# Optimization experiments

Measured on AMD Instinct MI355X. Metric: run time of the kernel, lower is better.

## Reference

```python
import jax, jax.numpy as jnp
import numpy as np

W_BLEND, L1, L2, L3 = 0.5, 0.3, 0.3, 0.4
B, S, F, H, C = 64, 256, 256, 1024, 256


def setup_inputs() -> dict:
    key = jax.random.key(0)
    ks = jax.random.split(key, 11)
    sc = 0.05  # keep recurrence numerically tame
    return {
        "x": jax.random.normal(ks[0], (B, S, F), jnp.float32),
        "W_ih0": jax.random.normal(ks[1], (4 * H, 2 * F), jnp.float32) * sc,
        "W_hh0": jax.random.normal(ks[2], (4 * H, H), jnp.float32) * sc,
        "b_ih0": jax.random.normal(ks[3], (4 * H,), jnp.float32) * sc,
        "b_hh0": jax.random.normal(ks[4], (4 * H,), jnp.float32) * sc,
        "W_ih1": jax.random.normal(ks[5], (4 * H, H), jnp.float32) * sc,
        "W_hh1": jax.random.normal(ks[6], (4 * H, H), jnp.float32) * sc,
        "b_ih1": jax.random.normal(ks[7], (4 * H,), jnp.float32) * sc,
        "b_hh1": jax.random.normal(ks[8], (4 * H,), jnp.float32) * sc,
        "fc_W": jax.random.normal(ks[9], (C, H), jnp.float32) * sc,
        "fc_b": jax.random.normal(ks[10], (C,), jnp.float32) * sc,
    }


def _lstm_cell(inp, h, c, W_ih, W_hh, b_ih, b_hh):
    # PyTorch gate order: i, f, g, o
    gates = inp @ W_ih.T + h @ W_hh.T + b_ih + b_hh  # [B, 4H]
    i, f, g, o = jnp.split(gates, 4, axis=-1)
    i, f, o = jax.nn.sigmoid(i), jax.nn.sigmoid(f), jax.nn.sigmoid(o)
    g = jnp.tanh(g)
    c_new = f * c + i * g
    h_new = o * jnp.tanh(c_new)
    return h_new, c_new


def reference(x, W_ih0, W_hh0, b_ih0, b_hh0, W_ih1, W_hh1, b_ih1, b_hh1, fc_W, fc_b):
    Bx = x.shape[0]
    denom = 1.0 + W_BLEND * (L1 + L2 + L3)
    h0 = jnp.zeros((Bx, H), x.dtype)
    c0 = jnp.zeros((Bx, H), x.dtype)
    action0 = jnp.zeros((Bx, F), x.dtype)

    def step(carry, inputs):
        h0_, c0_, h1_, c1_, action = carry
        x_t, idx = inputs  # x_t: [B, F]
        inp = jnp.concatenate([x_t, action], axis=-1)  # [B, 2F]
        h0n, c0n = _lstm_cell(inp, h0_, c0_, W_ih0, W_hh0, b_ih0, b_hh0)
        h1n, c1n = _lstm_cell(h0n, h1_, c1_, W_ih1, W_hh1, b_ih1, b_hh1)
        out = h1n @ fc_W.T + fc_b  # [B, C] == [B, F]
        blend = ((1.0 + W_BLEND * L2) * x_t + W_BLEND * L1 * action
                 + W_BLEND * L3 * out) / denom
        new_action = jnp.where(idx < 1, x_t, blend)
        return (h0n, c0n, h1n, c1n, new_action), new_action

    xs = (jnp.swapaxes(x, 0, 1), jnp.arange(x.shape[1]))  # ([S,B,F], [S])
    _, actions = jax.lax.scan(step, (h0, c0, h0, c0, action0), xs)
    return jnp.swapaxes(actions, 0, 1)  # [B, S, F]
```

## Files before the change

kernel.cpp:

```cpp
#include <hip/hip_runtime.h>

#define B_ 64
#define S_ 256
#define F_ 256
#define H_ 1024

typedef __attribute__((ext_vector_type(8))) short bf16x8;
typedef __attribute__((ext_vector_type(4))) float f32x4;
typedef unsigned long long u64;

#define MFMA(a, b, c) __builtin_amdgcn_mfma_f32_16x16x32_bf16(a, b, c, 0, 0, 0)
#define CBAR() asm volatile("" ::: "memory")

__device__ __forceinline__ float sig(float v) { return 1.0f / (1.0f + __expf(-v)); }
__device__ __forceinline__ float tanh_(float v) { return 1.0f - 2.0f / (__expf(2.0f * v) + 1.0f); }
__device__ __forceinline__ short bfr(float f) {
    unsigned u = __float_as_uint(f);
    u += 0x7fffu + ((u >> 16) & 1u);
    return (short)(u >> 16);
}

__device__ __forceinline__ void st4(short* base, size_t byteoff, unsigned v) {
    __hip_atomic_store((unsigned*)((char*)base + byteoff), v,
                       __ATOMIC_RELAXED, __HIP_MEMORY_SCOPE_AGENT);
}

__device__ __forceinline__ void flag_add(unsigned* line) {
    asm volatile("s_waitcnt vmcnt(0)" ::: "memory");
    __hip_atomic_fetch_add(line, 1u, __ATOMIC_RELAXED, __HIP_MEMORY_SCOPE_AGENT);
}

__device__ __forceinline__ void flag_wait_g(unsigned* lines, int lane31, unsigned tgt) {
    for (;;) {
        unsigned s = __hip_atomic_load(&lines[lane31 * 16], __ATOMIC_RELAXED,
                                       __HIP_MEMORY_SCOPE_AGENT);
        s += __shfl_xor(s, 1);
        s += __shfl_xor(s, 2);
        s += __shfl_xor(s, 4);
        s += __shfl_xor(s, 8);
        s += __shfl_xor(s, 16);
        if (s >= tgt) break;
        __builtin_amdgcn_s_sleep(1);
    }
    CBAR();
}

__device__ __forceinline__ void rel_wait(unsigned* f, unsigned tgt) {
    while (__hip_atomic_load(f, __ATOMIC_RELAXED, __HIP_MEMORY_SCOPE_AGENT) < tgt)
        __builtin_amdgcn_s_sleep(1);
    CBAR();
}

__device__ __forceinline__ void tok_spin(volatile unsigned* tk, unsigned v) {
    while (*tk < v) __builtin_amdgcn_s_sleep(1);
    CBAR();
}

__global__ __launch_bounds__(256) void conv_x(const float* __restrict__ x,
                                              short* __restrict__ xbf) {
    int tid = blockIdx.x * 256 + threadIdx.x;
    int lane = tid & 63;
    int m = (tid >> 6) & 3;
    int kf = (tid >> 8) & 7;
    int t = tid >> 11;
    int b = m * 16 + (lane & 15);
    int kb = kf * 32 + (lane >> 4) * 8;
    const float* src = x + ((size_t)b * S_ + t) * F_ + kb;
    float4 v0 = *(const float4*)src, v1 = *(const float4*)(src + 4);
    bf16x8 o;
    o[0] = bfr(v0.x); o[1] = bfr(v0.y); o[2] = bfr(v0.z); o[3] = bfr(v0.w);
    o[4] = bfr(v1.x); o[5] = bfr(v1.y); o[6] = bfr(v1.z); o[7] = bfr(v1.w);
    *(bf16x8*)(xbf + (size_t)tid * 8) = o;
}

__global__ void zero_f(float* __restrict__ p, int n) {
    int i = blockIdx.x * blockDim.x + threadIdx.x;
    if (i < n) p[i] = 0.0f;
}

__global__ __launch_bounds__(256) void precomp(const float* __restrict__ Wih0,
                                               const float* __restrict__ fcW,
                                               const float* __restrict__ fcb,
                                               short* __restrict__ Mf,
                                               float* __restrict__ c0ws) {
    __shared__ float WaL[16][256];
    const int nf = blockIdx.x, tid = threadIdx.x;
    #pragma unroll
    for (int r = 0; r < 16; ++r) {
        int rowp = nf * 16 + r;
        int up = rowp >> 2, gat = rowp & 3;
        WaL[r][tid] = Wih0[(size_t)(gat * H_ + up) * 512 + 256 + tid];
    }
    __syncthreads();
    f32x4 acc[16];
    #pragma unroll
    for (int r = 0; r < 16; ++r) acc[r] = (f32x4){0, 0, 0, 0};
    for (int c = 0; c < 256; ++c) {
        f32x4 wv = *(const f32x4*)&fcW[(size_t)c * 1024 + tid * 4];
        #pragma unroll
        for (int r = 0; r < 16; ++r) acc[r] += WaL[r][c] * wv;
    }
    #pragma unroll
    for (int r = 0; r < 16; ++r) {
        #pragma unroll
        for (int jj = 0; jj < 4; ++jj) {
            int h = tid * 4 + jj;
            int kf = h >> 5;
            int lane = r + ((h >> 3) & 3) * 16;
            int j = h & 7;
            Mf[((size_t)nf * 32 + kf) * 512 + lane * 8 + j] = bfr(acc[r][jj]);
        }
    }
    if (tid < 16) {
        float s = 0.0f;
        for (int c = 0; c < 256; ++c) s += WaL[tid][c] * fcb[c];
        c0ws[nf * 16 + tid] = s;
    }
}

#define GATES(v)                                                        \
    float x1 = __shfl_xor((v), 1), x2 = __shfl_xor((v), 2), x3 = __shfl_xor((v), 3); \
    float aL = g1 ? x1 : (v), aH = g1 ? x3 : x2;                        \
    float bL = g1 ? (v) : x1, bH = g1 ? x2 : x3;                        \
    float i_ = g2 ? aH : aL;                                            \
    float f_ = g2 ? bH : bL;                                            \
    float gc = g2 ? aL : aH;                                            \
    float o_ = g2 ? bL : bH;                                            \
    i_ = sig(i_); f_ = sig(f_); o_ = sig(o_); gc = tanh_(gc);

__global__ __launch_bounds__(512, 1) void persist(
    const float* __restrict__ Wih0, const float* __restrict__ Whh0,
    const float* __restrict__ bih0, const float* __restrict__ bhh0,
    const float* __restrict__ Wih1, const float* __restrict__ Whh1,
    const float* __restrict__ bih1, const float* __restrict__ bhh1,
    const float* __restrict__ fcW,  const float* __restrict__ fcb,
    const float* __restrict__ x,    const short* __restrict__ xbf,
    short* __restrict__ h0S, short* __restrict__ h1S,
    const short* __restrict__ Mf, const float* __restrict__ c0ws,
    float* __restrict__ outp,
    unsigned* __restrict__ flagA, unsigned* __restrict__ flagB,
    unsigned* __restrict__ relA,  unsigned* __restrict__ relB)
{
    __shared__ f32x4 redGA[2048];
    __shared__ f32x4 redBv[2048];
    __shared__ f32x4 redDv[2048];
    __shared__ f32x4 fcF[256];
    __shared__ short ldsC[16384];
    __shared__ unsigned tokA, tokB;
    const int tid = threadIdx.x, lane = tid & 63, w = tid >> 6;
    const int nf = blockIdx.x;
    const int lane31 = lane & 31;
    unsigned* lineA = &flagA[(nf >> 3) * 16];
    unsigned* lineB = &flagB[(nf >> 3) * 16];
    unsigned* myRelA = &relA[(nf >> 5) * 16];
    unsigned* myRelB = &relB[(nf >> 5) * 16];
    const int rowp = nf * 16 + (lane & 15);
    const int up = rowp >> 2, g = rowp & 3;
    const int g1 = lane & 1, g2 = lane & 2;
    const f32x4 zero4 = {0, 0, 0, 0};
    const int chunkA = (nf >> 3) * 4 + w;
    const int lsBase = ((nf & 7) >> 1) * 16;
    const int pb = (nf & 1) * 4 + ((lane & 15) >> 3) * 2;
    const int mfc = nf >> 4;

    if (tid == 0) { tokA = 0; tokB = 0; }

    bf16x8 wA0, waQ, wH[8], wX[8];
    {
        int k = w * 32 + (lane >> 4) * 8;
        const float* src = Wih0 + (size_t)(g * H_ + up) * 512 + k;
        #pragma unroll
        for (int j = 0; j < 8; ++j) wA0[j] = bfr(src[j]);
    }
    {
        int k = 256 + w * 32 + (lane >> 4) * 8;
        const float* src = Wih0 + (size_t)(g * H_ + up) * 512 + k;
        #pragma unroll
        for (int j = 0; j < 8; ++j) waQ[j] = bfr(src[j]);
    }
    if (w < 4) {
        #pragma unroll
        for (int i = 0; i < 8; ++i) {
            int k = (w * 8 + i) * 32 + (lane >> 4) * 8;
            const float* sh = Whh0 + (size_t)(g * H_ + up) * 1024 + k;
            const float* sx = Wih1 + (size_t)(g * H_ + up) * 1024 + k;
            #pragma unroll
            for (int j = 0; j < 8; ++j) { wH[i][j] = bfr(sh[j]); wX[i][j] = bfr(sx[j]); }
        }
    } else {
        #pragma unroll
        for (int i = 0; i < 8; ++i) {
            int k = ((w - 4) * 8 + i) * 32 + (lane >> 4) * 8;
            const float* sh = Whh1 + (size_t)(g * H_ + up) * 1024 + k;
            #pragma unroll
            for (int j = 0; j < 8; ++j) wH[i][j] = bfr(sh[j]);
            wX[i] = *(const bf16x8*)(Mf + ((size_t)nf * 32 + (w - 4) * 8 + i) * 512 + lane * 8);
        }
    }
    const float bias0 = bih0[g * H_ + up] + bhh0[g * H_ + up];
    const float bias1 = bih1[g * H_ + up] + bhh1[g * H_ + up];
    const float c0l = c0ws[nf * 16 + (lane & 15)];
    float biasC = 0.0f;
    if (nf < 64) {
        int rowc = (nf & 15) * 16 + (lane & 15);
        biasC = fcb[rowc];
        #pragma unroll
        for (int i = 0; i < 4; ++i) {
            int kf = w * 4 + i;
            int k = kf * 32 + (lane >> 4) * 8;
            const float* src = fcW + (size_t)rowc * 1024 + k;
            short* d = ldsC + ((size_t)kf * 64 + lane) * 8;
            #pragma unroll
            for (int j = 0; j < 8; ++j) d[j] = bfr(src[j]);
        }
    }
    __syncthreads();

    float cs0[4] = {0, 0, 0, 0}, cs1[4] = {0, 0, 0, 0};
    float areg[4] = {0, 0, 0, 0}, P[4] = {0, 0, 0, 0};

    f32x4 ga0, ga1, ga2, ga3, q0, q1, q2, q3;
    f32x4 qp0 = zero4, qp1 = zero4, qp2 = zero4, qp3 = zero4;
    {
        const short* p = xbf + (size_t)w * 2048 + lane * 8;
        bf16x8 a0 = *(const bf16x8*)(p);
        bf16x8 a1 = *(const bf16x8*)(p + 512);
        bf16x8 a2 = *(const bf16x8*)(p + 1024);
        bf16x8 a3 = *(const bf16x8*)(p + 1536);
        ga0 = MFMA(a0, wA0, zero4);  ga1 = MFMA(a1, wA0, zero4);
        ga2 = MFMA(a2, wA0, zero4);  ga3 = MFMA(a3, wA0, zero4);
        q0 = MFMA(a0, waQ, zero4);  q1 = MFMA(a1, waQ, zero4);
        q2 = MFMA(a2, waQ, zero4);  q3 = MFMA(a3, waQ, zero4);
    }

    for (int t = 0; t < S_; ++t) {
        const unsigned ut = (unsigned)t;
        short* h0w = h0S + (size_t)t * 65536;
        const short* h1r = h1S + (size_t)t * 65536;
        short* h1w = h1S + (size_t)(t + 1) * 65536;

        if (w == 0) {
            if (t > 0) {
                if (nf == 0) {
                    flag_wait_g(flagB, lane31, 256u * ut);
                    if (lane < 8)
                        __hip_atomic_store(&relB[lane * 16], ut,
                                           __ATOMIC_RELAXED, __HIP_MEMORY_SCOPE_AGENT);
                } else {
                    rel_wait(myRelB, ut);
                }
                if (lane == 0) *(volatile unsigned*)&tokB = ut;
                CBAR();
            }
        } else if (w >= 4 && t > 0) {
            tok_spin(&tokB, ut);
        }
        redGA[(w * 4 + 0) * 64 + lane] = ga0;
        redGA[(w * 4 + 1) * 64 + lane] = ga1;
        redGA[(w * 4 + 2) * 64 + lane] = ga2;
        redGA[(w * 4 + 3) * 64 + lane] = ga3;
        f32x4 m0 = zero4, m1 = zero4, m2 = zero4, m3 = zero4;
        if (w >= 4) {
            f32x4 b0 = zero4, b1 = zero4, b2 = zero4, b3 = zero4;
            #pragma unroll
            for (int i = 0; i < 8; ++i) {
                const short* p = h1r + (size_t)((w - 4) * 8 + i) * 2048 + lane * 8;
                bf16x8 a0 = *(const bf16x8*)(p);
                bf16x8 a1 = *(const bf16x8*)(p + 512);
                bf16x8 a2 = *(const bf16x8*)(p + 1024);
                bf16x8 a3 = *(const bf16x8*)(p + 1536);
                if (t > 1) {
                    m0 = MFMA(a0, wX[i], m0);
                    m1 = MFMA(a1, wX[i], m1);
                    m2 = MFMA(a2, wX[i], m2);
                    m3 = MFMA(a3, wX[i], m3);
                }
                b0 = MFMA(a0, wH[i], b0);
                b1 = MFMA(a1, wH[i], b1);
                b2 = MFMA(a2, wH[i], b2);
                b3 = MFMA(a3, wH[i], b3);
            }
            redBv[(w * 4 + 0) * 64 + lane] = b0;
            redBv[(w * 4 + 1) * 64 + lane] = b1;
            redBv[(w * 4 + 2) * 64 + lane] = b2;
            redBv[(w * 4 + 3) * 64 + lane] = b3;
        }
        if (t > 0) {
            f32x4 R0, R1, R2, R3;
            if (t == 1) { R0 = qp0; R1 = qp1; R2 = qp2; R3 = qp3; }
            else if (w >= 4) {
                R0 = 1.15f * qp0 + 0.2f * m0;
                R1 = 1.15f * qp1 + 0.2f * m1;
                R2 = 1.15f * qp2 + 0.2f * m2;
                R3 = 1.15f * qp3 + 0.2f * m3;
            } else {
                R0 = 1.15f * qp0; R1 = 1.15f * qp1; R2 = 1.15f * qp2; R3 = 1.15f * qp3;
            }
            redDv[(w * 4 + 0) * 64 + lane] = R0;
            redDv[(w * 4 + 1) * 64 + lane] = R1;
            redDv[(w * 4 + 2) * 64 + lane] = R2;
            redDv[(w * 4 + 3) * 64 + lane] = R3;
        }
        __syncthreads();

        if (w < 4) {
            if (t > 0) {
                f32x4 sD = redDv[(0 * 4 + w) * 64 + lane];
                #pragma unroll
                for (int k = 1; k < 8; ++k) sD += redDv[(k * 4 + w) * 64 + lane];
                #pragma unroll
                for (int r = 0; r < 4; ++r)
                    P[r] = (t == 1) ? sD[r]
                         : (sD[r] + 0.15f * P[r] + 0.2f * c0l) * (1.0f / 1.5f);
            }
            f32x4 s = redGA[(0 * 4 + w) * 64 + lane];
            #pragma unroll
            for (int k = 1; k < 8; ++k) s += redGA[(k * 4 + w) * 64 + lane];
            #pragma unroll
            for (int r = 0; r < 4; ++r) {
                float v = s[r] + bias0 + P[r];
                GATES(v)
                float cn = f_ * cs0[r] + i_ * gc;
                cs0[r] = cn;
                float hn = o_ * tanh_(cn);
                int hv = (int)(unsigned short)bfr(hn);
                int ot = __shfl_xor(hv, 4);
                unsigned p32 = (lane & 4) ? (unsigned)((ot & 0xffff) | (hv << 16))
                                          : (unsigned)((hv & 0xffff) | (ot << 16));
                if ((lane & 7) == 0) {
                    int b = w * 16 + (lane >> 4) * 4 + r;
                    int ls = lsBase + (b & 15);
                    st4(h0w, (size_t)chunkA * 1024 + (size_t)ls * 16 + pb * 2, p32);
                }
            }
        } else if (nf < 64 && t > 0) {
            const int j = w - 4;
            f32x4 f0 = zero4;
            #pragma unroll
            for (int i = 0; i < 8; ++i) {
                const int kf = j * 8 + i;
                const bf16x8 bw = *(const bf16x8*)(ldsC + ((size_t)kf * 64 + lane) * 8);
                bf16x8 a = *(const bf16x8*)(h1r + (size_t)kf * 2048 + (size_t)mfc * 512 + lane * 8);
                f0 = MFMA(a, bw, f0);
            }
            fcF[j * 64 + lane] = f0;
        }
        __syncthreads();
        if (tid == 0) flag_add(lineA);

        if (w == 0) {
            if (nf == 0) {
                flag_wait_g(flagA, lane31, 256u * (ut + 1u));
                if (lane < 8)
                    __hip_atomic_store(&relA[lane * 16], ut + 1u,
                                       __ATOMIC_RELAXED, __HIP_MEMORY_SCOPE_AGENT);
            } else {
                rel_wait(myRelA, ut + 1u);
            }
            if (lane == 0) *(volatile unsigned*)&tokA = ut + 1u;
            CBAR();
        } else if (w < 4) {
            tok_spin(&tokA, ut + 1u);
        } else if (w == 4 && nf < 64 && t > 0) {
            f32x4 s = fcF[lane];
            s += fcF[64 + lane];
            s += fcF[128 + lane];
            s += fcF[192 + lane];
            const int c = (nf & 15) * 16 + (lane & 15);
            #pragma unroll
            for (int r = 0; r < 4; ++r) {
                float ov = s[r] + biasC;
                int b = mfc * 16 + (lane >> 4) * 4 + r;
                size_t xi = ((size_t)b * S_ + (t - 1)) * F_ + c;
                float xv = x[xi];
                float na = (t == 1) ? xv
                         : (1.15f * xv + 0.15f * areg[r] + 0.2f * ov) * (1.0f / 1.5f);
                areg[r] = na;
                outp[xi] = na;
            }
        }

        if (w < 4) {
            f32x4 b0 = zero4, b1 = zero4, b2 = zero4, b3 = zero4;
            ga0 = zero4; ga1 = zero4; ga2 = zero4; ga3 = zero4;
            #pragma unroll
            for (int i = 0; i < 8; ++i) {
                const short* p = h0w + (size_t)(w * 8 + i) * 2048 + lane * 8;
                bf16x8 a0 = *(const bf16x8*)(p);
                bf16x8 a1 = *(const bf16x8*)(p + 512);
                bf16x8 a2 = *(const bf16x8*)(p + 1024);
                bf16x8 a3 = *(const bf16x8*)(p + 1536);
                b0 = MFMA(a0, wX[i], b0);
                b1 = MFMA(a1, wX[i], b1);
                b2 = MFMA(a2, wX[i], b2);
                b3 = MFMA(a3, wX[i], b3);
                ga0 = MFMA(a0, wH[i], ga0);
                ga1 = MFMA(a1, wH[i], ga1);
                ga2 = MFMA(a2, wH[i], ga2);
                ga3 = MFMA(a3, wH[i], ga3);
            }
            redBv[(w * 4 + 0) * 64 + lane] = b0;
            redBv[(w * 4 + 1) * 64 + lane] = b1;
            redBv[(w * 4 + 2) * 64 + lane] = b2;
            redBv[(w * 4 + 3) * 64 + lane] = b3;
        }
        __syncthreads();

        if (w < 4) {
            f32x4 s = redBv[(0 * 4 + w) * 64 + lane];
            #pragma unroll
            for (int k = 1; k < 8; ++k) s += redBv[(k * 4 + w) * 64 + lane];
            #pragma unroll
            for (int r = 0; r < 4; ++r) {
                float v = s[r] + bias1;
                GATES(v)
                float cn = f_ * cs1[r] + i_ * gc;
                cs1[r] = cn;
                float hn = o_ * tanh_(cn);
                int hv = (int)(unsigned short)bfr(hn);
                int ot = __shfl_xor(hv, 4);
                unsigned p32 = (lane & 4) ? (unsigned)((ot & 0xffff) | (hv << 16))
                                          : (unsigned)((hv & 0xffff) | (ot << 16));
                if ((lane & 7) == 0) {
                    int b = w * 16 + (lane >> 4) * 4 + r;
                    int ls = lsBase + (b & 15);
                    st4(h1w, (size_t)chunkA * 1024 + (size_t)ls * 16 + pb * 2, p32);
                }
            }
        }
        __syncthreads();
        if (tid == 0) flag_add(lineB);

        if (t < S_ - 1) {
            qp0 = q0; qp1 = q1; qp2 = q2; qp3 = q3;
            const short* p = xbf + (size_t)(t + 1) * 16384 + (size_t)w * 2048 + lane * 8;
            bf16x8 a0 = *(const bf16x8*)(p);
            bf16x8 a1 = *(const bf16x8*)(p + 512);
            bf16x8 a2 = *(const bf16x8*)(p + 1024);
            bf16x8 a3 = *(const bf16x8*)(p + 1536);
            ga0 = MFMA(a0, wA0, (w < 4) ? ga0 : zero4);
            ga1 = MFMA(a1, wA0, (w < 4) ? ga1 : zero4);
            ga2 = MFMA(a2, wA0, (w < 4) ? ga2 : zero4);
            ga3 = MFMA(a3, wA0, (w < 4) ? ga3 : zero4);
            q0 = MFMA(a0, waQ, zero4);  q1 = MFMA(a1, waQ, zero4);
            q2 = MFMA(a2, waQ, zero4);  q3 = MFMA(a3, waQ, zero4);
        }
    }

    if (w == 0) {
        if (nf == 0) {
            flag_wait_g(flagB, lane31, 256u * 256u);
            if (lane < 8)
                __hip_atomic_store(&relB[lane * 16], 256u,
                                   __ATOMIC_RELAXED, __HIP_MEMORY_SCOPE_AGENT);
        } else {
            rel_wait(myRelB, 256u);
        }
        if (lane == 0) *(volatile unsigned*)&tokB = 256u;
        CBAR();
    } else if (w >= 4) {
        tok_spin(&tokB, 256u);
    }
    if (nf < 64) {
        const short* h1f = h1S + (size_t)256 * 65536;
        if (w >= 4) {
            const int j = w - 4;
            f32x4 f0 = zero4;
            #pragma unroll
            for (int i = 0; i < 8; ++i) {
                const int kf = j * 8 + i;
                const bf16x8 bw = *(const bf16x8*)(ldsC + ((size_t)kf * 64 + lane) * 8);
                bf16x8 a = *(const bf16x8*)(h1f + (size_t)kf * 2048 + (size_t)mfc * 512 + lane * 8);
                f0 = MFMA(a, bw, f0);
            }
            fcF[j * 64 + lane] = f0;
        }
        __syncthreads();
        if (w == 4) {
            f32x4 s = fcF[lane];
            s += fcF[64 + lane];
            s += fcF[128 + lane];
            s += fcF[192 + lane];
            const int c = (nf & 15) * 16 + (lane & 15);
            #pragma unroll
            for (int r = 0; r < 4; ++r) {
                float ov = s[r] + biasC;
                int b = mfc * 16 + (lane >> 4) * 4 + r;
                size_t xi = ((size_t)b * S_ + (S_ - 1)) * F_ + c;
                float xv = x[xi];
                float na = (1.15f * xv + 0.15f * areg[r] + 0.2f * ov) * (1.0f / 1.5f);
                outp[xi] = na;
            }
        }
    }
}

extern "C" void kernel_launch(void* const* d_in, const int* in_sizes, int n_in,
                              void* d_out, int out_size, void* d_ws, size_t ws_size,
                              hipStream_t stream) {
    const float* x    = (const float*)d_in[0];
    const float* Wih0 = (const float*)d_in[1];
    const float* Whh0 = (const float*)d_in[2];
    const float* bih0 = (const float*)d_in[3];
    const float* bhh0 = (const float*)d_in[4];
    const float* Wih1 = (const float*)d_in[5];
    const float* Whh1 = (const float*)d_in[6];
    const float* bih1 = (const float*)d_in[7];
    const float* bhh1 = (const float*)d_in[8];
    const float* fcW  = (const float*)d_in[9];
    const float* fcb  = (const float*)d_in[10];
    float* outp = (float*)d_out;

    char* ws = (char*)d_ws;
    short* xbf   = (short*)(ws + 0);
    short* Mf    = (short*)(ws + 8388608);
    float* c0ws  = (float*)(ws + 16777216);
    unsigned* flagA = (unsigned*)(ws + 16793600);
    unsigned* flagB = (unsigned*)(ws + 16795648);
    unsigned* relA  = (unsigned*)(ws + 16797696);
    unsigned* relB  = (unsigned*)(ws + 16798208);
    short* h0S   = (short*)(ws + 16798720);
    short* h1S   = (short*)(ws + 50353152);

    conv_x<<<2048, 256, 0, stream>>>(x, xbf);
    precomp<<<256, 256, 0, stream>>>(Wih0, fcW, fcb, Mf, c0ws);
    zero_f<<<5, 256, 0, stream>>>((float*)(ws + 16793600), 1280);
    zero_f<<<128, 256, 0, stream>>>((float*)(ws + 50353152), 32768);

    persist<<<256, 512, 0, stream>>>(Wih0, Whh0, bih0, bhh0,
                                     Wih1, Whh1, bih1, bhh1,
                                     fcW, fcb, x, xbf,
                                     h0S, h1S, Mf, c0ws, outp,
                                     flagA, flagB, relA, relB);
}
```

Measured before the change: 3.317 ms.

## Split per-step grid barriers into lo/hi halves to overlap MFMA with sync

Replaces the single per-step grid-wide flag barrier for each layer with two half-batch barriers (lo and hi), each counted from wave-level arrivals through an LDS counter. Consumers can then start MFMAs on the first batch half while the second half's release is still pending. The aim is to hide part of the cross-block synchronisation latency in this persistent recurrent kernel. In exchange it adds twice as many flag lines, spin waits and atomics, and the new ordering and flag accounting carry some correctness risk.

```diff
diff --git a/kernel.cpp b/kernel.cpp
--- a/kernel.cpp
+++ b/kernel.cpp
@@ -25,9 +25,14 @@
                        __ATOMIC_RELAXED, __HIP_MEMORY_SCOPE_AGENT);
 }
 
-__device__ __forceinline__ void flag_add(unsigned* line) {
+__device__ __forceinline__ void arrive2(unsigned* cnt_lds, unsigned* line, int lane, unsigned step) {
     asm volatile("s_waitcnt vmcnt(0)" ::: "memory");
-    __hip_atomic_fetch_add(line, 1u, __ATOMIC_RELAXED, __HIP_MEMORY_SCOPE_AGENT);
+    if (lane == 0) {
+        unsigned old = __hip_atomic_fetch_add(cnt_lds, 1u, __ATOMIC_RELAXED,
+                                              __HIP_MEMORY_SCOPE_WORKGROUP);
+        if (old == 2u * step + 1u)
+            __hip_atomic_fetch_add(line, 1u, __ATOMIC_RELAXED, __HIP_MEMORY_SCOPE_AGENT);
+    }
 }
 
 __device__ __forceinline__ void flag_wait_g(unsigned* lines, int lane31, unsigned tgt) {
@@ -43,6 +48,14 @@
         __builtin_amdgcn_s_sleep(1);
     }
     CBAR();
+}
+
+__device__ __forceinline__ void master_release(unsigned* lines, unsigned* rel,
+                                               int lane, int lane31,
+                                               unsigned tgt, unsigned val) {
+    flag_wait_g(lines, lane31, tgt);
+    if (lane < 8)
+        __hip_atomic_store(&rel[lane * 16], val, __ATOMIC_RELAXED, __HIP_MEMORY_SCOPE_AGENT);
 }
 
 __device__ __forceinline__ void rel_wait(unsigned* f, unsigned tgt) {
@@ -138,22 +151,29 @@
     short* __restrict__ h0S, short* __restrict__ h1S,
     const short* __restrict__ Mf, const float* __restrict__ c0ws,
     float* __restrict__ outp,
-    unsigned* __restrict__ flagA, unsigned* __restrict__ flagB,
-    unsigned* __restrict__ relA,  unsigned* __restrict__ relB)
+    unsigned* __restrict__ flagAlo, unsigned* __restrict__ flagAhi,
+    unsigned* __restrict__ flagBlo, unsigned* __restrict__ flagBhi,
+    unsigned* __restrict__ relAlo,  unsigned* __restrict__ relAhi,
+    unsigned* __restrict__ relBlo,  unsigned* __restrict__ relBhi)
 {
     __shared__ f32x4 redGA[2048];
     __shared__ f32x4 redBv[2048];
     __shared__ f32x4 redDv[2048];
     __shared__ f32x4 fcF[256];
     __shared__ short ldsC[16384];
-    __shared__ unsigned tokA, tokB;
+    __shared__ unsigned tokAlo, tokAhi, tokBlo, tokBhi;
+    __shared__ unsigned cA[2], cB[2];
     const int tid = threadIdx.x, lane = tid & 63, w = tid >> 6;
     const int nf = blockIdx.x;
     const int lane31 = lane & 31;
-    unsigned* lineA = &flagA[(nf >> 3) * 16];
-    unsigned* lineB = &flagB[(nf >> 3) * 16];
-    unsigned* myRelA = &relA[(nf >> 5) * 16];
-    unsigned* myRelB = &relB[(nf >> 5) * 16];
+    unsigned* lineAlo = &flagAlo[(nf >> 3) * 16];
+    unsigned* lineAhi = &flagAhi[(nf >> 3) * 16];
+    unsigned* lineBlo = &flagBlo[(nf >> 3) * 16];
+    unsigned* lineBhi = &flagBhi[(nf >> 3) * 16];
+    unsigned* myRelAlo = &relAlo[(nf >> 5) * 16];
+    unsigned* myRelAhi = &relAhi[(nf >> 5) * 16];
+    unsigned* myRelBlo = &relBlo[(nf >> 5) * 16];
+    unsigned* myRelBhi = &relBhi[(nf >> 5) * 16];
     const int rowp = nf * 16 + (lane & 15);
     const int up = rowp >> 2, g = rowp & 3;
     const int g1 = lane & 1, g2 = lane & 2;
@@ -163,7 +183,10 @@
     const int pb = (nf & 1) * 4 + ((lane & 15) >> 3) * 2;
     const int mfc = nf >> 4;
 
-    if (tid == 0) { tokA = 0; tokB = 0; }
+    if (tid == 0) {
+        tokAlo = 0; tokAhi = 0; tokBlo = 0; tokBhi = 0;
+        cA[0] = 0; cA[1] = 0; cB[0] = 0; cB[1] = 0;
+    }
 
     bf16x8 wA0, waQ, wH[8], wX[8];
     {
@@ -239,21 +262,22 @@
         const short* h1r = h1S + (size_t)t * 65536;
         short* h1w = h1S + (size_t)(t + 1) * 65536;
 
-        if (w == 0) {
-            if (t > 0) {
-                if (nf == 0) {
-                    flag_wait_g(flagB, lane31, 256u * ut);
-                    if (lane < 8)
-                        __hip_atomic_store(&relB[lane * 16], ut,
-                                           __ATOMIC_RELAXED, __HIP_MEMORY_SCOPE_AGENT);
-                } else {
-                    rel_wait(myRelB, ut);
-                }
-                if (lane == 0) *(volatile unsigned*)&tokB = ut;
-                CBAR();
-            }
-        } else if (w >= 4 && t > 0) {
-            tok_spin(&tokB, ut);
+        if (w == 0 && t > 0) {
+            if (nf == 0) {
+                master_release(flagBlo, relBlo, lane, lane31, 256u * ut, ut);
+                if (lane == 0) *(volatile unsigned*)&tokBlo = ut;
+                CBAR();
+                master_release(flagBhi, relBhi, lane, lane31, 256u * ut, ut);
+                if (lane == 0) *(volatile unsigned*)&tokBhi = ut;
+                CBAR();
+            } else {
+                rel_wait(myRelBlo, ut);
+                if (lane == 0) *(volatile unsigned*)&tokBlo = ut;
+                CBAR();
+                rel_wait(myRelBhi, ut);
+                if (lane == 0) *(volatile unsigned*)&tokBhi = ut;
+                CBAR();
+            }
         }
         redGA[(w * 4 + 0) * 64 + lane] = ga0;
         redGA[(w * 4 + 1) * 64 + lane] = ga1;
@@ -262,21 +286,29 @@
         f32x4 m0 = zero4, m1 = zero4, m2 = zero4, m3 = zero4;
         if (w >= 4) {
             f32x4 b0 = zero4, b1 = zero4, b2 = zero4, b3 = zero4;
+            if (t > 0) tok_spin(&tokBlo, ut);
             #pragma unroll
             for (int i = 0; i < 8; ++i) {
                 const short* p = h1r + (size_t)((w - 4) * 8 + i) * 2048 + lane * 8;
                 bf16x8 a0 = *(const bf16x8*)(p);
                 bf16x8 a1 = *(const bf16x8*)(p + 512);
+                if (t > 1) {
+                    m0 = MFMA(a0, wX[i], m0);
+                    m1 = MFMA(a1, wX[i], m1);
+                }
+                b0 = MFMA(a0, wH[i], b0);
+                b1 = MFMA(a1, wH[i], b1);
+            }
+            if (t > 0) tok_spin(&tokBhi, ut);
+            #pragma unroll
+            for (int i = 0; i < 8; ++i) {
+                const short* p = h1r + (size_t)((w - 4) * 8 + i) * 2048 + lane * 8;
                 bf16x8 a2 = *(const bf16x8*)(p + 1024);
                 bf16x8 a3 = *(const bf16x8*)(p + 1536);
                 if (t > 1) {
-                    m0 = MFMA(a0, wX[i], m0);
-                    m1 = MFMA(a1, wX[i], m1);
                     m2 = MFMA(a2, wX[i], m2);
                     m3 = MFMA(a3, wX[i], m3);
                 }
-                b0 = MFMA(a0, wH[i], b0);
-                b1 = MFMA(a1, wH[i], b1);
                 b2 = MFMA(a2, wH[i], b2);
                 b3 = MFMA(a3, wH[i], b3);
             }
@@ -333,6 +365,7 @@
                     st4(h0w, (size_t)chunkA * 1024 + (size_t)ls * 16 + pb * 2, p32);
                 }
             }
+            arrive2(&cA[w >> 1], (w >> 1) ? lineAhi : lineAlo, lane, ut);
         } else if (nf < 64 && t > 0) {
             const int j = w - 4;
             f32x4 f0 = zero4;
@@ -346,22 +379,8 @@
             fcF[j * 64 + lane] = f0;
         }
         __syncthreads();
-        if (tid == 0) flag_add(lineA);
-
-        if (w == 0) {
-            if (nf == 0) {
-                flag_wait_g(flagA, lane31, 256u * (ut + 1u));
-                if (lane < 8)
-                    __hip_atomic_store(&relA[lane * 16], ut + 1u,
-                                       __ATOMIC_RELAXED, __HIP_MEMORY_SCOPE_AGENT);
-            } else {
-                rel_wait(myRelA, ut + 1u);
-            }
-            if (lane == 0) *(volatile unsigned*)&tokA = ut + 1u;
-            CBAR();
-        } else if (w < 4) {
-            tok_spin(&tokA, ut + 1u);
-        } else if (w == 4 && nf < 64 && t > 0) {
+
+        if (w == 4 && nf < 64 && t > 0) {
             f32x4 s = fcF[lane];
             s += fcF[64 + lane];
             s += fcF[128 + lane];
@@ -379,23 +398,51 @@
                 outp[xi] = na;
             }
         }
-
+        if (w == 0) {
+            if (nf == 0) {
+                master_release(flagAlo, relAlo, lane, lane31, 256u * (ut + 1u), ut + 1u);
+                if (lane == 0) *(volatile unsigned*)&tokAlo = ut + 1u;
+                CBAR();
+                master_release(flagAhi, relAhi, lane, lane31, 256u * (ut + 1u), ut + 1u);
+                if (lane == 0) *(volatile unsigned*)&tokAhi = ut + 1u;
+                CBAR();
+            } else {
+                rel_wait(myRelAlo, ut + 1u);
+                if (lane == 0) *(volatile unsigned*)&tokAlo = ut + 1u;
+                CBAR();
+            }
+        }
         if (w < 4) {
             f32x4 b0 = zero4, b1 = zero4, b2 = zero4, b3 = zero4;
+            if (w != 0) tok_spin(&tokAlo, ut + 1u);
             ga0 = zero4; ga1 = zero4; ga2 = zero4; ga3 = zero4;
             #pragma unroll
             for (int i = 0; i < 8; ++i) {
                 const short* p = h0w + (size_t)(w * 8 + i) * 2048 + lane * 8;
                 bf16x8 a0 = *(const bf16x8*)(p);
                 bf16x8 a1 = *(const bf16x8*)(p + 512);
+                b0 = MFMA(a0, wX[i], b0);
+                b1 = MFMA(a1, wX[i], b1);
+                ga0 = MFMA(a0, wH[i], ga0);
+                ga1 = MFMA(a1, wH[i], ga1);
+            }
+            if (w == 0) {
+                if (nf == 0) {
+                } else {
+                    rel_wait(myRelAhi, ut + 1u);
+                    if (lane == 0) *(volatile unsigned*)&tokAhi = ut + 1u;
+                    CBAR();
+                }
+            } else {
+                tok_spin(&tokAhi, ut + 1u);
+            }
+            #pragma unroll
+            for (int i = 0; i < 8; ++i) {
+                const short* p = h0w + (size_t)(w * 8 + i) * 2048 + lane * 8;
                 bf16x8 a2 = *(const bf16x8*)(p + 1024);
                 bf16x8 a3 = *(const bf16x8*)(p + 1536);
-                b0 = MFMA(a0, wX[i], b0);
-                b1 = MFMA(a1, wX[i], b1);
                 b2 = MFMA(a2, wX[i], b2);
                 b3 = MFMA(a3, wX[i], b3);
-                ga0 = MFMA(a0, wH[i], ga0);
-                ga1 = MFMA(a1, wH[i], ga1);
                 ga2 = MFMA(a2, wH[i], ga2);
                 ga3 = MFMA(a3, wH[i], ga3);
             }
@@ -427,9 +474,9 @@
                     st4(h1w, (size_t)chunkA * 1024 + (size_t)ls * 16 + pb * 2, p32);
                 }
             }
+            arrive2(&cB[w >> 1], (w >> 1) ? lineBhi : lineBlo, lane, ut);
         }
         __syncthreads();
-        if (tid == 0) flag_add(lineB);
 
         if (t < S_ - 1) {
             qp0 = q0; qp1 = q1; qp2 = q2; qp3 = q3;
@@ -449,17 +496,16 @@
 
     if (w == 0) {
         if (nf == 0) {
-            flag_wait_g(flagB, lane31, 256u * 256u);
-            if (lane < 8)
-                __hip_atomic_store(&relB[lane * 16], 256u,
-                                   __ATOMIC_RELAXED, __HIP_MEMORY_SCOPE_AGENT);
+            master_release(flagBlo, relBlo, lane, lane31, 256u * 256u, 256u);
+            master_release(flagBhi, relBhi, lane, lane31, 256u * 256u, 256u);
         } else {
-            rel_wait(myRelB, 256u);
-        }
-        if (lane == 0) *(volatile unsigned*)&tokB = 256u;
+            rel_wait(myRelBlo, 256u);
+            rel_wait(myRelBhi, 256u);
+        }
+        if (lane == 0) { *(volatile unsigned*)&tokBlo = 256u; *(volatile unsigned*)&tokBhi = 256u; }
         CBAR();
     } else if (w >= 4) {
-        tok_spin(&tokB, 256u);
+        tok_spin(&tokBhi, 256u);
     }
     if (nf < 64) {
         const short* h1f = h1S + (size_t)256 * 65536;
@@ -515,21 +561,26 @@
     short* xbf   = (short*)(ws + 0);
     short* Mf    = (short*)(ws + 8388608);
     float* c0ws  = (float*)(ws + 16777216);
-    unsigned* flagA = (unsigned*)(ws + 16793600);
-    unsigned* flagB = (unsigned*)(ws + 16795648);
-    unsigned* relA  = (unsigned*)(ws + 16797696);
-    unsigned* relB  = (unsigned*)(ws + 16798208);
-    short* h0S   = (short*)(ws + 16798720);
-    short* h1S   = (short*)(ws + 50353152);
+    unsigned* flagAlo = (unsigned*)(ws + 16793600);
+    unsigned* flagAhi = (unsigned*)(ws + 16795648);
+    unsigned* flagBlo = (unsigned*)(ws + 16797696);
+    unsigned* flagBhi = (unsigned*)(ws + 16799744);
+    unsigned* relAlo  = (unsigned*)(ws + 16801792);
+    unsigned* relAhi  = (unsigned*)(ws + 16802304);
+    unsigned* relBlo  = (unsigned*)(ws + 16802816);
+    unsigned* relBhi  = (unsigned*)(ws + 16803328);
+    short* h0S   = (short*)(ws + 16803840);
+    short* h1S   = (short*)(ws + 50358272);
 
     conv_x<<<2048, 256, 0, stream>>>(x, xbf);
     precomp<<<256, 256, 0, stream>>>(Wih0, fcW, fcb, Mf, c0ws);
-    zero_f<<<5, 256, 0, stream>>>((float*)(ws + 16793600), 1280);
-    zero_f<<<128, 256, 0, stream>>>((float*)(ws + 50353152), 32768);
+    zero_f<<<10, 256, 0, stream>>>((float*)(ws + 16793600), 2560);
+    zero_f<<<128, 256, 0, stream>>>((float*)(ws + 50358272), 32768);
 
     persist<<<256, 512, 0, stream>>>(Wih0, Whh0, bih0, bhh0,
                                      Wih1, Whh1, bih1, bhh1,
                                      fcW, fcb, x, xbf,
                                      h0S, h1S, Mf, c0ws, outp,
-                                     flagA, flagB, relA, relB);
-}
+                                     flagAlo, flagAhi, flagBlo, flagBhi,
+                                     relAlo, relAhi, relBlo, relBhi);
+}
```

Measured after the change: 4.416 ms. +33.1%, slower.
